# Optimization experiments

Measured on AMD Instinct MI355X. Metric: run time of the kernel, lower is better.

## Reference

```python
import jax, jax.numpy as jnp
import numpy as np

B, C, N = 64, 512, 3000
GH, GW = 90, 50          # coordinate grid the points are sampled from
MAX_H, MAX_W = 70, 40    # module max_height / max_width
N_VALID = 2800           # points per sample with ys > -1


def setup_inputs() -> dict:
    key = jax.random.key(0)
    kf, kp = jax.random.split(key)
    features = jax.random.normal(kf, (B, C, N), dtype=jnp.float32)
    # unique grid cells per batch item -> no duplicate scatter targets
    perms = jax.vmap(lambda k: jax.random.permutation(k, GH * GW)[:N])(
        jax.random.split(kp, B))  # (B, N)
    ys = (perms // GW).astype(jnp.int32)
    xs = (perms % GW).astype(jnp.int32)
    valid = jnp.arange(N) < N_VALID
    ys = jnp.where(valid[None, :], ys, -1)  # invalid points marked ys == -1
    return {"features": features, "ys": ys, "xs": xs}


def reference(features, ys, xs):
    # Eval-mode (validation=True) forward: deterministic centered crop/pad.
    mask = ys > -1  # (B, N) real points
    BIG = 1_000_000
    min_y = jnp.where(mask, ys, BIG).min(axis=1)
    min_x = jnp.where(mask, xs, BIG).min(axis=1)
    max_y = jnp.where(mask, ys, -BIG).max(axis=1)
    max_x = jnp.where(mask, xs, -BIG).max(axis=1)
    h = max_y - min_y + 1
    w = max_x - min_x + 1
    swap = w > h  # transpose tmp map when wider than tall
    H0 = jnp.where(swap, w, h)
    W0 = jnp.where(swap, h, w)
    # per-point coords inside the (possibly transposed) tmp map
    r = jnp.where(swap[:, None], xs - min_x[:, None], ys - min_y[:, None])
    c = jnp.where(swap[:, None], ys - min_y[:, None], xs - min_x[:, None])
    h_dif = H0 - MAX_H
    w_dif = W0 - MAX_W
    cut_top = jnp.where(h_dif > 0, (h_dif + 1) // 2, 0)   # ceil(h_dif/2)
    pad_top = jnp.where(h_dif > 0, 0, (-h_dif + 1) // 2)  # ceil(-h_dif/2)
    cut_left = jnp.where(w_dif > 0, (w_dif + 1) // 2, 0)
    # NOTE: original passes (pad_right, pad_left, ...) to F.pad, so the
    # computed 'pad_right' = ceil(-w_dif/2) is applied as LEFT padding.
    left_pad = jnp.where(w_dif > 0, 0, (-w_dif + 1) // 2)
    rr = r - cut_top[:, None] + pad_top[:, None]
    cc = c - cut_left[:, None] + left_pad[:, None]
    in_bounds = mask & (rr >= 0) & (rr < MAX_H) & (cc >= 0) & (cc < MAX_W)
    rr = jnp.where(in_bounds, rr, MAX_H)  # push cropped/invalid points OOB
    cc = jnp.where(in_bounds, cc, MAX_W)
    canvas = jnp.full((B, C, MAX_H, MAX_W), -1.0, dtype=features.dtype)
    bi = jnp.arange(B)[:, None]  # (B, 1)
    # scatter: canvas[b, :, rr[b,n], cc[b,n]] = features[b, :, n]
    canvas = canvas.at[bi, :, rr, cc].set(jnp.swapaxes(features, 1, 2),
                                          mode="drop")
    real2d = jnp.all(canvas != -1.0, axis=1)  # (B, H, W)
    # f_map is zeros (use_dummy_feature=False): blend = mask * canvas
    return jnp.where(real2d[:, None, :, :], canvas, jnp.zeros((), features.dtype))
```

## Files before the change

### kernel.cpp

```cpp
#include <hip/hip_runtime.h>
#include <stdint.h>

#define NB 64
#define NC 512
#define NPTS 3000
#define MAXH 70
#define MAXW 40
#define HW (MAXH * MAXW)
#define THREADS 256
#define CPB 32
#define NV4 750
#define NV4P 768
#define OV4 (HW / 4)
#define FIXCAP 8192

typedef float f32x4 __attribute__((ext_vector_type(4)));

__device__ __forceinline__ void gload_lds16(const void* g, void* l) {
    __builtin_amdgcn_global_load_lds(
        (const __attribute__((address_space(1))) uint32_t*)g,
        (__attribute__((address_space(3))) uint32_t*)l,
        16, 0, 0);
}

__global__ void fm_zero_cnt(int* cnt) {
    if (threadIdx.x == 0) cnt[0] = 0;
}

__launch_bounds__(THREADS)
__global__ void fm_gather_kernel(const float* __restrict__ feat,
                                 const int* __restrict__ ys,
                                 const int* __restrict__ xs,
                                 float* __restrict__ out,
                                 int* __restrict__ fix_cnt,
                                 int* __restrict__ fix_list,
                                 int fix_cap)
{
    __shared__ float4 tb[3][NV4P];
    __shared__ int    s_red[16];
    __shared__ int    s_par[5];

    const int blocks_per_b = NC / CPB;
    const int b   = blockIdx.x / blocks_per_b;
    const int c0  = (blockIdx.x % blocks_per_b) * CPB;
    const int tid = threadIdx.x;
    const int lane = tid & 63;
    const int w    = tid >> 6;

    const int* ysb = ys + b * NPTS;
    const int* xsb = xs + b * NPTS;
    int* ybuf = (int*)tb[0];
    int* xbuf = (int*)tb[1];
    int* inv  = (int*)tb[2];

    int vminY = 0x7fffffff, vminX = 0x7fffffff;
    int vmaxY = -0x7fffffff, vmaxX = -0x7fffffff;
    for (int i = tid; i < NV4; i += THREADS) {
        int4 ya = ((const int4*)ysb)[i];
        int4 xa = ((const int4*)xsb)[i];
        ((int4*)ybuf)[i] = ya;
        ((int4*)xbuf)[i] = xa;
        int yv[4] = {ya.x, ya.y, ya.z, ya.w};
        int xv[4] = {xa.x, xa.y, xa.z, xa.w};
#pragma unroll
        for (int j = 0; j < 4; ++j) {
            if (yv[j] > -1) {
                vminY = min(vminY, yv[j]); vmaxY = max(vmaxY, yv[j]);
                vminX = min(vminX, xv[j]); vmaxX = max(vmaxX, xv[j]);
            }
        }
    }
    for (int i = tid; i < HW; i += THREADS) inv[i] = -1;
#pragma unroll
    for (int off = 32; off > 0; off >>= 1) {
        vminY = min(vminY, __shfl_xor(vminY, off));
        vmaxY = max(vmaxY, __shfl_xor(vmaxY, off));
        vminX = min(vminX, __shfl_xor(vminX, off));
        vmaxX = max(vmaxX, __shfl_xor(vmaxX, off));
    }
    if (lane == 0) {
        s_red[w]      = vminY;
        s_red[4  + w] = vmaxY;
        s_red[8  + w] = vminX;
        s_red[12 + w] = vmaxX;
    }
    __syncthreads();
    if (tid == 0) {
        int mnY = min(min(s_red[0], s_red[1]),   min(s_red[2],  s_red[3]));
        int mxY = max(max(s_red[4], s_red[5]),   max(s_red[6],  s_red[7]));
        int mnX = min(min(s_red[8], s_red[9]),   min(s_red[10], s_red[11]));
        int mxX = max(max(s_red[12], s_red[13]), max(s_red[14], s_red[15]));
        int h  = mxY - mnY + 1;
        int w_ = mxX - mnX + 1;
        int swap = (w_ > h) ? 1 : 0;
        int H0 = swap ? w_ : h;
        int W0 = swap ? h : w_;
        int h_dif = H0 - MAXH;
        int w_dif = W0 - MAXW;
        int cut_top  = (h_dif > 0) ? (h_dif + 1) / 2 : 0;
        int pad_top  = (h_dif > 0) ? 0 : (-h_dif + 1) / 2;
        int cut_left = (w_dif > 0) ? (w_dif + 1) / 2 : 0;
        int left_pad = (w_dif > 0) ? 0 : (-w_dif + 1) / 2;
        s_par[0] = swap;
        s_par[1] = mnY;
        s_par[2] = mnX;
        s_par[3] = pad_top - cut_top;
        s_par[4] = left_pad - cut_left;
    }
    __syncthreads();

    {
        const int swp = s_par[0], mnY = s_par[1], mnX = s_par[2];
        const int roff = s_par[3], coff = s_par[4];
        for (int n = tid; n < NPTS; n += THREADS) {
            int y = ybuf[n];
            int x = xbuf[n];
            if (y > -1) {
                int r  = swp ? (x - mnX) : (y - mnY);
                int cl = swp ? (y - mnY) : (x - mnX);
                int rr = r + roff;
                int cc = cl + coff;
                if (rr >= 0 && rr < MAXH && cc >= 0 && cc < MAXW)
                    inv[rr * MAXW + cc] = n;
            }
        }
    }
    __syncthreads();

    int nreg[3][4];
#pragma unroll
    for (int it = 0; it < 3; ++it) {
        int i4 = it * THREADS + tid;
        if (i4 < OV4) {
#pragma unroll
            for (int j = 0; j < 4; ++j) nreg[it][j] = inv[i4 * 4 + j];
        }
    }
    __syncthreads();

    {
        const float4* src = (const float4*)(feat + (size_t)(b * NC + c0) * NPTS);
#pragma unroll
        for (int it = 0; it < 3; ++it) {
            int i = it * THREADS + tid;
            int s = (i < NV4) ? i : (NV4 - 1);
            gload_lds16(src + s, tb[0] + i);
        }
    }

    int cur = 0;
    for (int ci = 0; ci < CPB; ++ci) {
        const int nxt = (cur == 2) ? 0 : cur + 1;
        if (ci + 1 < CPB) {
            const float4* src =
                (const float4*)(feat + (size_t)(b * NC + c0 + ci + 1) * NPTS);
            float4* bn = tb[nxt];
#pragma unroll
            for (int it = 0; it < 3; ++it) {
                int i = it * THREADS + tid;
                int s = (i < NV4) ? i : (NV4 - 1);
                gload_lds16(src + s, bn + i);
            }
        }
        if (ci == 0) {
            asm volatile("s_waitcnt vmcnt(3)" ::: "memory");
        } else if (ci + 1 < CPB) {
            asm volatile("s_waitcnt vmcnt(5)" ::: "memory");
        } else {
            asm volatile("s_waitcnt vmcnt(2)" ::: "memory");
        }
        __builtin_amdgcn_sched_barrier(0);
        __builtin_amdgcn_s_barrier();
        __builtin_amdgcn_sched_barrier(0);

        const float* fp = (const float*)tb[cur];
        f32x4* orow = (f32x4*)(out + (size_t)(b * NC + c0 + ci) * HW);
#pragma unroll
        for (int it = 0; it < 3; ++it) {
            int i4 = it * THREADS + tid;
            if (i4 < OV4) {
                f32x4 v;
#pragma unroll
                for (int j = 0; j < 4; ++j) {
                    int n = nreg[it][j];
                    float val = 0.0f;
                    if (n >= 0) {
                        val = fp[n];
                        if (val == -1.0f) {
                            int pos = atomicAdd(fix_cnt, 1);
                            if (pos < fix_cap) fix_list[pos] = b * HW + i4 * 4 + j;
                        }
                    }
                    v[j] = val;
                }
                __builtin_nontemporal_store(v, &orow[i4]);
            }
        }
        cur = nxt;
    }
}

__global__ void fm_fixup_kernel(const int* __restrict__ fix_cnt,
                                const int* __restrict__ fix_list,
                                int fix_cap,
                                float* __restrict__ out)
{
    int count = min(fix_cnt[0], fix_cap);
    long total = (long)count * NC;
    long stride = (long)gridDim.x * blockDim.x;
    for (long t = (long)blockIdx.x * blockDim.x + threadIdx.x; t < total; t += stride) {
        int e = (int)(t / NC);
        int c = (int)(t % NC);
        int cell = fix_list[e];
        int b   = cell / HW;
        int pos = cell % HW;
        __builtin_nontemporal_store(0.0f, &out[(size_t)(b * NC + c) * HW + pos]);
    }
}

extern "C" void kernel_launch(void* const* d_in, const int* in_sizes, int n_in,
                              void* d_out, int out_size, void* d_ws, size_t ws_size,
                              hipStream_t stream) {
    const float* feat = (const float*)d_in[0];
    const int*   ys   = (const int*)d_in[1];
    const int*   xs   = (const int*)d_in[2];
    float* out = (float*)d_out;

    int* fix_cnt  = (int*)d_ws;
    int* fix_list = (int*)((char*)d_ws + 16);
    int fix_cap = 0;
    if (ws_size > 16) {
        size_t avail = (ws_size - 16) / 4;
        fix_cap = (int)((avail < FIXCAP) ? avail : FIXCAP);
    }

    fm_zero_cnt<<<1, 64, 0, stream>>>(fix_cnt);

    int grid = NB * (NC / CPB);
    fm_gather_kernel<<<grid, THREADS, 0, stream>>>(feat, ys, xs, out,
                                                   fix_cnt, fix_list, fix_cap);

    fm_fixup_kernel<<<128, 256, 0, stream>>>(fix_cnt, fix_list, fix_cap, out);
}
```

Before: 169.3 us.

## Precompute per-batch inverse index map in a separate kernel before gather

Adds a 64-block kernel that computes the bounding box, crop and pad offsets and the cell-to-point inverse map once per batch item, and writes it to workspace. A new gather kernel loads the map from global memory instead of repeating the ys/xs reduction and scatter in all 16 channel-blocks of each batch item. This shortens each gather block's prologue but adds a kernel launch and a serial dependency. The original monolithic path is kept as a fallback when the workspace is too small.

```diff
diff --git a/kernel.cpp b/kernel.cpp
--- a/kernel.cpp
+++ b/kernel.cpp
@@ -13,6 +13,8 @@
 #define NV4P 768
 #define OV4 (HW / 4)
 #define FIXCAP 8192
+#define WS_INV_OFF (16 + FIXCAP * 4)
+#define WS_NEED    (WS_INV_OFF + NB * HW * 4)
 
 typedef float f32x4 __attribute__((ext_vector_type(4)));
 
@@ -28,30 +30,23 @@
 }
 
 __launch_bounds__(THREADS)
-__global__ void fm_gather_kernel(const float* __restrict__ feat,
-                                 const int* __restrict__ ys,
-                                 const int* __restrict__ xs,
-                                 float* __restrict__ out,
-                                 int* __restrict__ fix_cnt,
-                                 int* __restrict__ fix_list,
-                                 int fix_cap)
+__global__ void fm_inv_kernel(const int* __restrict__ ys,
+                              const int* __restrict__ xs,
+                              int* __restrict__ invg)
 {
-    __shared__ float4 tb[3][NV4P];
-    __shared__ int    s_red[16];
-    __shared__ int    s_par[5];
-
-    const int blocks_per_b = NC / CPB;
-    const int b   = blockIdx.x / blocks_per_b;
-    const int c0  = (blockIdx.x % blocks_per_b) * CPB;
+    __shared__ int inv[HW];
+    __shared__ int ybuf[NPTS];
+    __shared__ int xbuf[NPTS];
+    __shared__ int s_red[16];
+    __shared__ int s_par[5];
+
+    const int b   = blockIdx.x;
     const int tid = threadIdx.x;
     const int lane = tid & 63;
     const int w    = tid >> 6;
 
     const int* ysb = ys + b * NPTS;
     const int* xsb = xs + b * NPTS;
-    int* ybuf = (int*)tb[0];
-    int* xbuf = (int*)tb[1];
-    int* inv  = (int*)tb[2];
 
     int vminY = 0x7fffffff, vminX = 0x7fffffff;
     int vmaxY = -0x7fffffff, vmaxX = -0x7fffffff;
@@ -108,7 +103,199 @@
         s_par[4] = left_pad - cut_left;
     }
     __syncthreads();
-
+    {
+        const int swp = s_par[0], mnY = s_par[1], mnX = s_par[2];
+        const int roff = s_par[3], coff = s_par[4];
+        for (int n = tid; n < NPTS; n += THREADS) {
+            int y = ybuf[n];
+            int x = xbuf[n];
+            if (y > -1) {
+                int r  = swp ? (x - mnX) : (y - mnY);
+                int cl = swp ? (y - mnY) : (x - mnX);
+                int rr = r + roff;
+                int cc = cl + coff;
+                if (rr >= 0 && rr < MAXH && cc >= 0 && cc < MAXW)
+                    inv[rr * MAXW + cc] = n;
+            }
+        }
+    }
+    __syncthreads();
+    int4* dst = (int4*)(invg + b * HW);
+    for (int i = tid; i < OV4; i += THREADS) dst[i] = ((const int4*)inv)[i];
+}
+
+__launch_bounds__(THREADS)
+__global__ void fm_gather_pre_kernel(const float* __restrict__ feat,
+                                     const int* __restrict__ invg,
+                                     float* __restrict__ out,
+                                     int* __restrict__ fix_cnt,
+                                     int* __restrict__ fix_list,
+                                     int fix_cap)
+{
+    __shared__ float4 tb[3][NV4P];
+
+    const int blocks_per_b = NC / CPB;
+    const int b   = blockIdx.x / blocks_per_b;
+    const int c0  = (blockIdx.x % blocks_per_b) * CPB;
+    const int tid = threadIdx.x;
+
+    int nreg[3][4];
+    {
+        const int4* src = (const int4*)(invg + b * HW);
+#pragma unroll
+        for (int it = 0; it < 3; ++it) {
+            int i4 = it * THREADS + tid;
+            if (i4 < OV4) {
+                int4 t = src[i4];
+                nreg[it][0] = t.x; nreg[it][1] = t.y;
+                nreg[it][2] = t.z; nreg[it][3] = t.w;
+            }
+        }
+    }
+
+    {
+        const float4* src = (const float4*)(feat + (size_t)(b * NC + c0) * NPTS);
+#pragma unroll
+        for (int it = 0; it < 3; ++it) {
+            int i = it * THREADS + tid;
+            int s = (i < NV4) ? i : (NV4 - 1);
+            gload_lds16(src + s, tb[0] + i);
+        }
+    }
+
+    int cur = 0;
+    for (int ci = 0; ci < CPB; ++ci) {
+        const int nxt = (cur == 2) ? 0 : cur + 1;
+        if (ci + 1 < CPB) {
+            const float4* src =
+                (const float4*)(feat + (size_t)(b * NC + c0 + ci + 1) * NPTS);
+            float4* bn = tb[nxt];
+#pragma unroll
+            for (int it = 0; it < 3; ++it) {
+                int i = it * THREADS + tid;
+                int s = (i < NV4) ? i : (NV4 - 1);
+                gload_lds16(src + s, bn + i);
+            }
+        }
+        if (ci == 0) {
+            asm volatile("s_waitcnt vmcnt(3)" ::: "memory");
+        } else if (ci + 1 < CPB) {
+            asm volatile("s_waitcnt vmcnt(5)" ::: "memory");
+        } else {
+            asm volatile("s_waitcnt vmcnt(2)" ::: "memory");
+        }
+        __builtin_amdgcn_sched_barrier(0);
+        __builtin_amdgcn_s_barrier();
+        __builtin_amdgcn_sched_barrier(0);
+
+        const float* fp = (const float*)tb[cur];
+        f32x4* orow = (f32x4*)(out + (size_t)(b * NC + c0 + ci) * HW);
+#pragma unroll
+        for (int it = 0; it < 3; ++it) {
+            int i4 = it * THREADS + tid;
+            if (i4 < OV4) {
+                f32x4 v;
+#pragma unroll
+                for (int j = 0; j < 4; ++j) {
+                    int n = nreg[it][j];
+                    float val = 0.0f;
+                    if (n >= 0) {
+                        val = fp[n];
+                        if (val == -1.0f) {
+                            int pos = atomicAdd(fix_cnt, 1);
+                            if (pos < fix_cap) fix_list[pos] = b * HW + i4 * 4 + j;
+                        }
+                    }
+                    v[j] = val;
+                }
+                __builtin_nontemporal_store(v, &orow[i4]);
+            }
+        }
+        cur = nxt;
+    }
+}
+
+__launch_bounds__(THREADS)
+__global__ void fm_gather_mono_kernel(const float* __restrict__ feat,
+                                      const int* __restrict__ ys,
+                                      const int* __restrict__ xs,
+                                      float* __restrict__ out,
+                                      int* __restrict__ fix_cnt,
+                                      int* __restrict__ fix_list,
+                                      int fix_cap)
+{
+    __shared__ float4 tb[3][NV4P];
+    __shared__ int    s_red[16];
+    __shared__ int    s_par[5];
+
+    const int blocks_per_b = NC / CPB;
+    const int b   = blockIdx.x / blocks_per_b;
+    const int c0  = (blockIdx.x % blocks_per_b) * CPB;
+    const int tid = threadIdx.x;
+    const int lane = tid & 63;
+    const int w    = tid >> 6;
+
+    const int* ysb = ys + b * NPTS;
+    const int* xsb = xs + b * NPTS;
+    int* ybuf = (int*)tb[0];
+    int* xbuf = (int*)tb[1];
+    int* inv  = (int*)tb[2];
+
+    int vminY = 0x7fffffff, vminX = 0x7fffffff;
+    int vmaxY = -0x7fffffff, vmaxX = -0x7fffffff;
+    for (int i = tid; i < NV4; i += THREADS) {
+        int4 ya = ((const int4*)ysb)[i];
+        int4 xa = ((const int4*)xsb)[i];
+        ((int4*)ybuf)[i] = ya;
+        ((int4*)xbuf)[i] = xa;
+        int yv[4] = {ya.x, ya.y, ya.z, ya.w};
+        int xv[4] = {xa.x, xa.y, xa.z, xa.w};
+#pragma unroll
+        for (int j = 0; j < 4; ++j) {
+            if (yv[j] > -1) {
+                vminY = min(vminY, yv[j]); vmaxY = max(vmaxY, yv[j]);
+                vminX = min(vminX, xv[j]); vmaxX = max(vmaxX, xv[j]);
+            }
+        }
+    }
+    for (int i = tid; i < HW; i += THREADS) inv[i] = -1;
+#pragma unroll
+    for (int off = 32; off > 0; off >>= 1) {
+        vminY = min(vminY, __shfl_xor(vminY, off));
+        vmaxY = max(vmaxY, __shfl_xor(vmaxY, off));
+        vminX = min(vminX, __shfl_xor(vminX, off));
+        vmaxX = max(vmaxX, __shfl_xor(vmaxX, off));
+    }
+    if (lane == 0) {
+        s_red[w]      = vminY;
+        s_red[4  + w] = vmaxY;
+        s_red[8  + w] = vminX;
+        s_red[12 + w] = vmaxX;
+    }
+    __syncthreads();
+    if (tid == 0) {
+        int mnY = min(min(s_red[0], s_red[1]),   min(s_red[2],  s_red[3]));
+        int mxY = max(max(s_red[4], s_red[5]),   max(s_red[6],  s_red[7]));
+        int mnX = min(min(s_red[8], s_red[9]),   min(s_red[10], s_red[11]));
+        int mxX = max(max(s_red[12], s_red[13]), max(s_red[14], s_red[15]));
+        int h  = mxY - mnY + 1;
+        int w_ = mxX - mnX + 1;
+        int swap = (w_ > h) ? 1 : 0;
+        int H0 = swap ? w_ : h;
+        int W0 = swap ? h : w_;
+        int h_dif = H0 - MAXH;
+        int w_dif = W0 - MAXW;
+        int cut_top  = (h_dif > 0) ? (h_dif + 1) / 2 : 0;
+        int pad_top  = (h_dif > 0) ? 0 : (-h_dif + 1) / 2;
+        int cut_left = (w_dif > 0) ? (w_dif + 1) / 2 : 0;
+        int left_pad = (w_dif > 0) ? 0 : (-w_dif + 1) / 2;
+        s_par[0] = swap;
+        s_par[1] = mnY;
+        s_par[2] = mnX;
+        s_par[3] = pad_top - cut_top;
+        s_par[4] = left_pad - cut_left;
+    }
+    __syncthreads();
     {
         const int swp = s_par[0], mnY = s_par[1], mnX = s_par[2];
         const int roff = s_par[3], coff = s_par[4];
@@ -228,17 +415,27 @@
 
     int* fix_cnt  = (int*)d_ws;
     int* fix_list = (int*)((char*)d_ws + 16);
-    int fix_cap = 0;
-    if (ws_size > 16) {
-        size_t avail = (ws_size - 16) / 4;
-        fix_cap = (int)((avail < FIXCAP) ? avail : FIXCAP);
-    }
 
     fm_zero_cnt<<<1, 64, 0, stream>>>(fix_cnt);
 
-    int grid = NB * (NC / CPB);
-    fm_gather_kernel<<<grid, THREADS, 0, stream>>>(feat, ys, xs, out,
-                                                   fix_cnt, fix_list, fix_cap);
-
-    fm_fixup_kernel<<<128, 256, 0, stream>>>(fix_cnt, fix_list, fix_cap, out);
-}
+    const int grid = NB * (NC / CPB);
+
+    if (ws_size >= (size_t)WS_NEED) {
+        int* invg = (int*)((char*)d_ws + WS_INV_OFF);
+        fm_inv_kernel<<<NB, THREADS, 0, stream>>>(ys, xs, invg);
+        fm_gather_pre_kernel<<<grid, THREADS, 0, stream>>>(feat, invg, out,
+                                                           fix_cnt, fix_list,
+                                                           FIXCAP);
+        fm_fixup_kernel<<<128, 256, 0, stream>>>(fix_cnt, fix_list, FIXCAP, out);
+    } else {
+        int fix_cap = 0;
+        if (ws_size > 16) {
+            size_t avail = (ws_size - 16) / 4;
+            fix_cap = (int)((avail < FIXCAP) ? avail : FIXCAP);
+        }
+        fm_gather_mono_kernel<<<grid, THREADS, 0, stream>>>(feat, ys, xs, out,
+                                                            fix_cnt, fix_list,
+                                                            fix_cap);
+        fm_fixup_kernel<<<128, 256, 0, stream>>>(fix_cnt, fix_list, fix_cap, out);
+    }
+}
```

New measurement: 169.5 us. About the same (+0.1%).
